# Kernel tuning notes

Hardware: AMD Instinct MI355X
Metric: run time of the kernel (lower is better)

## Reference

```python
import jax, jax.numpy as jnp
import numpy as np

N_NODES = 100000
N_EDGES = 1000000
IN_DIM = 64
OUT_DIM = 64


def setup_inputs() -> dict:
    key = jax.random.key(0)
    k1, k2, k3 = jax.random.split(key, 3)
    x = jax.random.normal(k1, (N_NODES, IN_DIM), dtype=jnp.float32)
    edge_index = jax.random.randint(k2, (2, N_EDGES), 0, N_NODES, dtype=jnp.int64)
    # PyG GCNConv linear weight [out_dim, in_dim] (glorot-ish scale) and bias
    W = jax.random.normal(k3, (OUT_DIM, IN_DIM), dtype=jnp.float32) * (1.0 / np.sqrt(IN_DIM))
    b = jnp.zeros((OUT_DIM,), dtype=jnp.float32)
    return {"x": x, "edge_index": edge_index, "W": W, "b": b}


def reference(x, edge_index, W, b):
    # GCNConv: add self-loops, symmetric deg^{-1/2} normalization,
    # linear transform, scatter-add aggregation, bias.
    # Dropout is identity in eval mode.
    N = x.shape[0]
    loop = jnp.arange(N, dtype=edge_index.dtype)
    src = jnp.concatenate([edge_index[0], loop])  # [E+N]
    dst = jnp.concatenate([edge_index[1], loop])  # [E+N]

    deg = jax.ops.segment_sum(jnp.ones_like(dst, dtype=x.dtype), dst, num_segments=N)
    dinv = jnp.where(deg > 0, jax.lax.rsqrt(deg), 0.0)  # [N]
    norm = dinv[src] * dinv[dst]                         # [E+N]

    h = x @ W.T                                          # [N, out_dim]
    msg = h[src] * norm[:, None]                         # gather + scale
    out = jax.ops.segment_sum(msg, dst, num_segments=N)  # scatter-add
    return out + b
```

## Files before the change

kernel.cpp:

```cpp
#include <hip/hip_runtime.h>

#define DIM 64
#define BIN_SHIFT 7
#define NODES_PER_BIN 128
#define MAX_BINS 1024
#define BIN_CAP 2048
#define CHUNK_EDGES 4096
#define SCATTER_THREADS 1024
#define GEMM_ROWS 128
#define FXSCALE 65536.0f
#define FXINV (1.0f / 65536.0f)
#define FXBIAS 524288u
#define MAGIC 12582912.0f
#define MAGIC_I 0x4B400000u
#define ACC_U64 33


using bf16x8 = __attribute__((ext_vector_type(8))) short;
using f32x4  = __attribute__((ext_vector_type(4))) float;

__device__ __forceinline__ unsigned short f2bf(float f) {
    unsigned u = __float_as_uint(f);
    u += 0x7fffu + ((u >> 16) & 1u);
    return (unsigned short)(u >> 16);
}
__device__ __forceinline__ float bf2f(unsigned short u) {
    return __uint_as_float((unsigned)u << 16);
}

__global__ __launch_bounds__(SCATTER_THREADS) void bin_scatter_kernel(
    const void* __restrict__ ei, int* __restrict__ gcur,
    int* __restrict__ pairs, int E, int nbins) {
    __shared__ int h1[MAX_BINS];
    __shared__ int base[MAX_BINS];
    __shared__ int s_notz;
    int tid = threadIdx.x;
    if (tid == 0) s_notz = 0;
    for (int i = tid; i < nbins; i += SCATTER_THREADS) h1[i] = 0;
    __syncthreads();
    if (((const int*)ei)[2 * tid + 1] != 0) s_notz = 1;
    __syncthreads();
    int is64 = (s_notz == 0);
    int chunk = blockIdx.x * CHUNK_EDGES;

    int ss[CHUNK_EDGES / SCATTER_THREADS], dd[CHUNK_EDGES / SCATTER_THREADS];
#pragma unroll
    for (int k = 0; k < CHUNK_EDGES / SCATTER_THREADS; ++k) {
        int i = chunk + k * SCATTER_THREADS + tid;
        if (i < E) {
            int s, d;
            if (is64) {
                s = (int)((const long long*)ei)[i];
                d = (int)((const long long*)ei)[(long long)i + E];
            } else {
                s = ((const int*)ei)[i];
                d = ((const int*)ei)[i + E];
            }
            ss[k] = s; dd[k] = d;
            atomicAdd(&h1[d >> BIN_SHIFT], 1);
        } else {
            dd[k] = -1;
        }
    }
    __syncthreads();
    for (int i = tid; i < nbins; i += SCATTER_THREADS) {
        int c = h1[i];
        base[i] = c ? (i * BIN_CAP + atomicAdd(&gcur[i], c)) : 0;
        h1[i] = 0;
    }
    __syncthreads();
#pragma unroll
    for (int k = 0; k < CHUNK_EDGES / SCATTER_THREADS; ++k) {
        if (dd[k] >= 0) {
            int bin = dd[k] >> BIN_SHIFT;
            int r = atomicAdd(&h1[bin], 1);
            int pos = base[bin] + r;
            if (pos < (bin + 1) * BIN_CAP)
                pairs[pos] = (ss[k] << BIN_SHIFT) | (dd[k] & (NODES_PER_BIN - 1));
        }
    }
}

__global__ __launch_bounds__(256) void deg_gemm_kernel(
    const float* __restrict__ x, const float* __restrict__ W,
    const int* __restrict__ pairs, const int* __restrict__ gcur,
    int* __restrict__ deg, float* __restrict__ dinv,
    unsigned short* __restrict__ h, int N) {
    __shared__ unsigned short Xs[GEMM_ROWS * 64];
    __shared__ unsigned short Ws[64 * 64];
    __shared__ int sdeg[NODES_PER_BIN];
    __shared__ float sdinv[NODES_PER_BIN];
    int tid = threadIdx.x;
    int b = blockIdx.x;
    int row0 = b << BIN_SHIFT;
    int nn = min(GEMM_ROWS, N - row0);
    int cntb = min(gcur[b], BIN_CAP);

    if (tid < NODES_PER_BIN) sdeg[tid] = 0;
#pragma unroll
    for (int u = 0; u < 2; ++u) {
        int idx = u * 256 + tid;
        int c = idx >> 3, k0 = (idx & 7) * 8;
        float4 a = *(const float4*)&W[c * 64 + k0];
        float4 bb = *(const float4*)&W[c * 64 + k0 + 4];
        bf16x8 v;
        v[0] = (short)f2bf(a.x); v[1] = (short)f2bf(a.y);
        v[2] = (short)f2bf(a.z); v[3] = (short)f2bf(a.w);
        v[4] = (short)f2bf(bb.x); v[5] = (short)f2bf(bb.y);
        v[6] = (short)f2bf(bb.z); v[7] = (short)f2bf(bb.w);
        int byteoff = c * 128 + ((k0 * 2) ^ ((c & 7) << 4));
        *(bf16x8*)((char*)Ws + byteoff) = v;
    }
    const float* xbase = x + (size_t)row0 * DIM;
#pragma unroll
    for (int u = 0; u < 4; ++u) {
        int idx = u * 256 + tid;
        int r = idx >> 3, k0 = (idx & 7) * 8;
        float4 a = make_float4(0.f, 0.f, 0.f, 0.f), bb = a;
        if (r < nn) {
            a = *(const float4*)&xbase[r * DIM + k0];
            bb = *(const float4*)&xbase[r * DIM + k0 + 4];
        }
        bf16x8 v;
        v[0] = (short)f2bf(a.x); v[1] = (short)f2bf(a.y);
        v[2] = (short)f2bf(a.z); v[3] = (short)f2bf(a.w);
        v[4] = (short)f2bf(bb.x); v[5] = (short)f2bf(bb.y);
        v[6] = (short)f2bf(bb.z); v[7] = (short)f2bf(bb.w);
        int byteoff = r * 128 + ((k0 * 2) ^ ((r & 7) << 4));
        *(bf16x8*)((char*)Xs + byteoff) = v;
    }
    __syncthreads();
    const int* pb = pairs + b * BIN_CAP;
    for (int i = tid; i < cntb; i += 256)
        atomicAdd(&sdeg[pb[i] & (NODES_PER_BIN - 1)], 1);
    __syncthreads();
    if (tid < NODES_PER_BIN) {
        int d = sdeg[tid];
        float dv = rsqrtf((float)(d + 1));
        sdinv[tid] = dv;
        if (tid < nn) {
            deg[row0 + tid] = d;
            dinv[row0 + tid] = dv;
        }
    }
    __syncthreads();

    int w = tid >> 6, l = tid & 63;
    int lm = l & 15, kg = l >> 4;
    f32x4 acc[2][4] = {};
#pragma unroll
    for (int ks = 0; ks < 2; ++ks) {
        int kbyte = ks * 64 + kg * 16;
        int r0g = 32 * w + lm;
        int r1g = 32 * w + 16 + lm;
        bf16x8 a0 = *(const bf16x8*)((const char*)Xs + r0g * 128 + (kbyte ^ ((r0g & 7) << 4)));
        bf16x8 a1 = *(const bf16x8*)((const char*)Xs + r1g * 128 + (kbyte ^ ((r1g & 7) << 4)));
#pragma unroll
        for (int nt = 0; nt < 4; ++nt) {
            int ng = nt * 16 + lm;
            bf16x8 bv = *(const bf16x8*)((const char*)Ws + ng * 128 + (kbyte ^ ((ng & 7) << 4)));
            acc[0][nt] = __builtin_amdgcn_mfma_f32_16x16x32_bf16(a0, bv, acc[0][nt], 0, 0, 0);
            acc[1][nt] = __builtin_amdgcn_mfma_f32_16x16x32_bf16(a1, bv, acc[1][nt], 0, 0, 0);
        }
    }
#pragma unroll
    for (int mt = 0; mt < 2; ++mt) {
#pragma unroll
        for (int j = 0; j < 4; ++j) {
            int rl = 32 * w + 16 * mt + (l >> 4) * 4 + j;
            if (rl < nn) {
                float dv = sdinv[rl];
                size_t rowoff = (size_t)(row0 + rl) * DIM;
#pragma unroll
                for (int nt = 0; nt < 4; ++nt)
                    h[rowoff + nt * 16 + lm] = f2bf(acc[mt][nt][j] * dv);
            }
        }
    }
}

__global__ __launch_bounds__(512) void aggregate_kernel(
    const unsigned short* __restrict__ h, const int* __restrict__ pairs,
    const int* __restrict__ gcur, const int* __restrict__ deg,
    const float* __restrict__ dinv, const float* __restrict__ bias,
    float* __restrict__ out, int N) {
    __shared__ unsigned long long acc[NODES_PER_BIN * ACC_U64];
    int b = blockIdx.x;
    int tid = threadIdx.x;
    int cnt = min(gcur[b], BIN_CAP);
    int node0 = b << BIN_SHIFT;
    int nn = min(NODES_PER_BIN, N - node0);

    for (int i = tid; i < NODES_PER_BIN * ACC_U64; i += 512) acc[i] = 0ULL;
    __syncthreads();

    int wave = tid >> 6, lane = tid & 63;
    int g = lane >> 4;
    int fq = lane & 15;
    const int* pb = pairs + b * BIN_CAP;
    int dummy = N << BIN_SHIFT;

    for (int j0 = 32 * wave; j0 < cnt; j0 += 256) {
        int pk[8]; bool vd[8];
#pragma unroll
        for (int u = 0; u < 8; ++u) {
            int e = j0 + 4 * u + g;
            vd[u] = (e < cnt);
            pk[u] = vd[u] ? pb[e] : dummy;
        }
        ushort4 r[8];
#pragma unroll
        for (int u = 0; u < 8; ++u)
            r[u] = *(const ushort4*)(h + (size_t)(pk[u] >> BIN_SHIFT) * DIM + 4 * fq);
#pragma unroll
        for (int u = 0; u < 8; ++u) {
            unsigned q0 = __float_as_uint(fmaf(bf2f(r[u].x), FXSCALE, MAGIC)) - (MAGIC_I - FXBIAS);
            unsigned q1 = __float_as_uint(fmaf(bf2f(r[u].y), FXSCALE, MAGIC)) - (MAGIC_I - FXBIAS);
            unsigned q2 = __float_as_uint(fmaf(bf2f(r[u].z), FXSCALE, MAGIC)) - (MAGIC_I - FXBIAS);
            unsigned q3 = __float_as_uint(fmaf(bf2f(r[u].w), FXSCALE, MAGIC)) - (MAGIC_I - FXBIAS);
            if (vd[u]) {
                unsigned long long* ar =
                    &acc[(pk[u] & (NODES_PER_BIN - 1)) * ACC_U64 + 2 * fq];
                atomicAdd(&ar[0], (unsigned long long)q0 | ((unsigned long long)q1 << 32));
                atomicAdd(&ar[1], (unsigned long long)q2 | ((unsigned long long)q3 << 32));
            }
        }
    }
    __syncthreads();

    const int* accd = (const int*)acc;
    float bl = bias[lane];
    for (int n0 = wave; n0 < nn; n0 += 8) {
        int gn = node0 + n0;
        int dgn = deg[gn];
        float di = dinv[gn];
        unsigned q = (unsigned)accd[n0 * (2 * ACC_U64) + lane];
        int sfx = (int)(q - (unsigned)dgn * FXBIAS);
        float sum = (float)sfx * FXINV;
        float self = bf2f(h[(size_t)gn * DIM + lane]);
        out[(size_t)gn * DIM + lane] = (sum + self) * di + bl;
    }
}

extern "C" void kernel_launch(void* const* d_in, const int* in_sizes, int n_in,
                              void* d_out, int out_size, void* d_ws, size_t ws_size,
                              hipStream_t stream) {
    const float* x = (const float*)d_in[0];
    const void* ei = d_in[1];
    const float* W = (const float*)d_in[2];
    const float* b = (const float*)d_in[3];
    float* out = (float*)d_out;

    int N = in_sizes[0] / DIM;
    int E = in_sizes[1] / 2;
    int nbins = (N + NODES_PER_BIN - 1) >> BIN_SHIFT;

    char* ws = (char*)d_ws;
    auto align256 = [](size_t v) { return (v + 255) & ~(size_t)255; };
    size_t off = 0;
    int* gcur = (int*)(ws + off);              off = align256(off + (size_t)MAX_BINS * 4);
    int* deg  = (int*)(ws + off);              off = align256(off + (size_t)(N + 1) * 4);
    float* dinv = (float*)(ws + off);          off = align256(off + (size_t)(N + 1) * 4);
    int* pairs = (int*)(ws + off);             off = align256(off + ((size_t)nbins * BIN_CAP + 64) * 4);
    unsigned short* h = (unsigned short*)(ws + off); off = align256(off + (size_t)(N + 1) * DIM * 2);

    int nchunks = (E + CHUNK_EDGES - 1) / CHUNK_EDGES;
    int gemmblocks = nbins;

    hipMemsetAsync(gcur, 0, (size_t)MAX_BINS * 4, stream);
    bin_scatter_kernel<<<nchunks, SCATTER_THREADS, 0, stream>>>(ei, gcur, pairs, E, nbins);
    deg_gemm_kernel<<<gemmblocks, 256, 0, stream>>>(x, W, pairs, gcur, deg, dinv, h, N);
    aggregate_kernel<<<nbins, 512, 0, stream>>>(h, pairs, gcur, deg, dinv, b, out, N);
}
```

Measured before the change: 128.6 us.

## Replace fixed-point LDS atomics with per-bin CSR sort and register accumulation

```diff
diff --git a/kernel.cpp b/kernel.cpp
--- a/kernel.cpp
+++ b/kernel.cpp
@@ -8,12 +8,7 @@
 #define CHUNK_EDGES 4096
 #define SCATTER_THREADS 1024
 #define GEMM_ROWS 128
-#define FXSCALE 65536.0f
-#define FXINV (1.0f / 65536.0f)
-#define FXBIAS 524288u
-#define MAGIC 12582912.0f
-#define MAGIC_I 0x4B400000u
-#define ACC_U64 33
+#define GCUR_STRIDE 16
 
 
 using bf16x8 = __attribute__((ext_vector_type(8))) short;
@@ -65,7 +60,7 @@
     __syncthreads();
     for (int i = tid; i < nbins; i += SCATTER_THREADS) {
         int c = h1[i];
-        base[i] = c ? (i * BIN_CAP + atomicAdd(&gcur[i], c)) : 0;
+        base[i] = c ? (i * BIN_CAP + atomicAdd(&gcur[i * GCUR_STRIDE], c)) : 0;
         h1[i] = 0;
     }
     __syncthreads();
@@ -84,7 +79,6 @@
 __global__ __launch_bounds__(256) void deg_gemm_kernel(
     const float* __restrict__ x, const float* __restrict__ W,
     const int* __restrict__ pairs, const int* __restrict__ gcur,
-    int* __restrict__ deg, float* __restrict__ dinv,
     unsigned short* __restrict__ h, int N) {
     __shared__ unsigned short Xs[GEMM_ROWS * 64];
     __shared__ unsigned short Ws[64 * 64];
@@ -94,7 +88,7 @@
     int b = blockIdx.x;
     int row0 = b << BIN_SHIFT;
     int nn = min(GEMM_ROWS, N - row0);
-    int cntb = min(gcur[b], BIN_CAP);
+    int cntb = min(gcur[b * GCUR_STRIDE], BIN_CAP);
 
     if (tid < NODES_PER_BIN) sdeg[tid] = 0;
 #pragma unroll
@@ -134,15 +128,8 @@
     for (int i = tid; i < cntb; i += 256)
         atomicAdd(&sdeg[pb[i] & (NODES_PER_BIN - 1)], 1);
     __syncthreads();
-    if (tid < NODES_PER_BIN) {
-        int d = sdeg[tid];
-        float dv = rsqrtf((float)(d + 1));
-        sdinv[tid] = dv;
-        if (tid < nn) {
-            deg[row0 + tid] = d;
-            dinv[row0 + tid] = dv;
-        }
-    }
+    if (tid < NODES_PER_BIN)
+        sdinv[tid] = rsqrtf((float)(sdeg[tid] + 1));
     __syncthreads();
 
     int w = tid >> 6, l = tid & 63;
@@ -181,64 +168,82 @@
 
 __global__ __launch_bounds__(512) void aggregate_kernel(
     const unsigned short* __restrict__ h, const int* __restrict__ pairs,
-    const int* __restrict__ gcur, const int* __restrict__ deg,
-    const float* __restrict__ dinv, const float* __restrict__ bias,
+    const int* __restrict__ gcur, const float* __restrict__ bias,
     float* __restrict__ out, int N) {
-    __shared__ unsigned long long acc[NODES_PER_BIN * ACC_U64];
+    __shared__ int rp[NODES_PER_BIN + 1];
+    __shared__ int cur[NODES_PER_BIN];
+    __shared__ int ssrc[BIN_CAP];
     int b = blockIdx.x;
     int tid = threadIdx.x;
-    int cnt = min(gcur[b], BIN_CAP);
+    int cnt = min(gcur[b * GCUR_STRIDE], BIN_CAP);
     int node0 = b << BIN_SHIFT;
     int nn = min(NODES_PER_BIN, N - node0);
 
-    for (int i = tid; i < NODES_PER_BIN * ACC_U64; i += 512) acc[i] = 0ULL;
-    __syncthreads();
-
-    int wave = tid >> 6, lane = tid & 63;
-    int g = lane >> 4;
-    int fq = lane & 15;
+    if (tid < NODES_PER_BIN) cur[tid] = 0;
+    __syncthreads();
     const int* pb = pairs + b * BIN_CAP;
-    int dummy = N << BIN_SHIFT;
-
-    for (int j0 = 32 * wave; j0 < cnt; j0 += 256) {
-        int pk[8]; bool vd[8];
-#pragma unroll
-        for (int u = 0; u < 8; ++u) {
-            int e = j0 + 4 * u + g;
-            vd[u] = (e < cnt);
-            pk[u] = vd[u] ? pb[e] : dummy;
-        }
-        ushort4 r[8];
-#pragma unroll
-        for (int u = 0; u < 8; ++u)
-            r[u] = *(const ushort4*)(h + (size_t)(pk[u] >> BIN_SHIFT) * DIM + 4 * fq);
-#pragma unroll
-        for (int u = 0; u < 8; ++u) {
-            unsigned q0 = __float_as_uint(fmaf(bf2f(r[u].x), FXSCALE, MAGIC)) - (MAGIC_I - FXBIAS);
-            unsigned q1 = __float_as_uint(fmaf(bf2f(r[u].y), FXSCALE, MAGIC)) - (MAGIC_I - FXBIAS);
-            unsigned q2 = __float_as_uint(fmaf(bf2f(r[u].z), FXSCALE, MAGIC)) - (MAGIC_I - FXBIAS);
-            unsigned q3 = __float_as_uint(fmaf(bf2f(r[u].w), FXSCALE, MAGIC)) - (MAGIC_I - FXBIAS);
-            if (vd[u]) {
-                unsigned long long* ar =
-                    &acc[(pk[u] & (NODES_PER_BIN - 1)) * ACC_U64 + 2 * fq];
-                atomicAdd(&ar[0], (unsigned long long)q0 | ((unsigned long long)q1 << 32));
-                atomicAdd(&ar[1], (unsigned long long)q2 | ((unsigned long long)q3 << 32));
-            }
-        }
-    }
-    __syncthreads();
-
-    const int* accd = (const int*)acc;
-    float bl = bias[lane];
-    for (int n0 = wave; n0 < nn; n0 += 8) {
-        int gn = node0 + n0;
-        int dgn = deg[gn];
-        float di = dinv[gn];
-        unsigned q = (unsigned)accd[n0 * (2 * ACC_U64) + lane];
-        int sfx = (int)(q - (unsigned)dgn * FXBIAS);
-        float sum = (float)sfx * FXINV;
-        float self = bf2f(h[(size_t)gn * DIM + lane]);
-        out[(size_t)gn * DIM + lane] = (sum + self) * di + bl;
+    int pk[4]; int np = 0;
+    for (int i = tid; i < cnt; i += 512) {
+        int p = pb[i];
+        pk[np++] = p;
+        atomicAdd(&cur[p & (NODES_PER_BIN - 1)], 1);
+    }
+    __syncthreads();
+    if (tid < NODES_PER_BIN) rp[tid + 1] = cur[tid];
+    if (tid == 0) rp[0] = 0;
+    __syncthreads();
+#pragma unroll
+    for (int s = 1; s < NODES_PER_BIN; s <<= 1) {
+        int v = 0;
+        if (tid < NODES_PER_BIN && tid >= s) v = rp[tid + 1 - s];
+        __syncthreads();
+        if (tid < NODES_PER_BIN && tid >= s) rp[tid + 1] += v;
+        __syncthreads();
+    }
+    if (tid < NODES_PER_BIN) cur[tid] = rp[tid];
+    __syncthreads();
+#pragma unroll 4
+    for (int k = 0; k < np; ++k) {
+        int r = atomicAdd(&cur[pk[k] & (NODES_PER_BIN - 1)], 1);
+        ssrc[r] = pk[k] >> BIN_SHIFT;
+    }
+    __syncthreads();
+
+    int grp = tid >> 4, fl = tid & 15;
+    float4 bl = *(const float4*)&bias[4 * fl];
+#pragma unroll 1
+    for (int k = 0; k < 4; ++k) {
+        int n = 4 * grp + k;
+        if (n >= nn) continue;
+        int s = rp[n], e = rp[n + 1];
+        float a0 = 0.f, a1 = 0.f, a2 = 0.f, a3 = 0.f;
+        int j = s;
+        for (; j + 4 <= e; j += 4) {
+            int s0 = ssrc[j], s1 = ssrc[j + 1], s2 = ssrc[j + 2], s3 = ssrc[j + 3];
+            ushort4 r0 = *(const ushort4*)(h + (size_t)s0 * DIM + 4 * fl);
+            ushort4 r1 = *(const ushort4*)(h + (size_t)s1 * DIM + 4 * fl);
+            ushort4 r2 = *(const ushort4*)(h + (size_t)s2 * DIM + 4 * fl);
+            ushort4 r3 = *(const ushort4*)(h + (size_t)s3 * DIM + 4 * fl);
+            a0 += (bf2f(r0.x) + bf2f(r1.x)) + (bf2f(r2.x) + bf2f(r3.x));
+            a1 += (bf2f(r0.y) + bf2f(r1.y)) + (bf2f(r2.y) + bf2f(r3.y));
+            a2 += (bf2f(r0.z) + bf2f(r1.z)) + (bf2f(r2.z) + bf2f(r3.z));
+            a3 += (bf2f(r0.w) + bf2f(r1.w)) + (bf2f(r2.w) + bf2f(r3.w));
+        }
+        for (; j < e; ++j) {
+            int s0 = ssrc[j];
+            ushort4 r0 = *(const ushort4*)(h + (size_t)s0 * DIM + 4 * fl);
+            a0 += bf2f(r0.x); a1 += bf2f(r0.y);
+            a2 += bf2f(r0.z); a3 += bf2f(r0.w);
+        }
+        int gn = node0 + n;
+        ushort4 sh = *(const ushort4*)(h + (size_t)gn * DIM + 4 * fl);
+        float di = rsqrtf((float)(e - s + 1));
+        float4 o;
+        o.x = (a0 + bf2f(sh.x)) * di + bl.x;
+        o.y = (a1 + bf2f(sh.y)) * di + bl.y;
+        o.z = (a2 + bf2f(sh.z)) * di + bl.z;
+        o.w = (a3 + bf2f(sh.w)) * di + bl.w;
+        *(float4*)&out[(size_t)gn * DIM + 4 * fl] = o;
     }
 }
 
@@ -258,17 +263,14 @@
     char* ws = (char*)d_ws;
     auto align256 = [](size_t v) { return (v + 255) & ~(size_t)255; };
     size_t off = 0;
-    int* gcur = (int*)(ws + off);              off = align256(off + (size_t)MAX_BINS * 4);
-    int* deg  = (int*)(ws + off);              off = align256(off + (size_t)(N + 1) * 4);
-    float* dinv = (float*)(ws + off);          off = align256(off + (size_t)(N + 1) * 4);
+    int* gcur = (int*)(ws + off);              off = align256(off + (size_t)MAX_BINS * GCUR_STRIDE * 4);
     int* pairs = (int*)(ws + off);             off = align256(off + ((size_t)nbins * BIN_CAP + 64) * 4);
     unsigned short* h = (unsigned short*)(ws + off); off = align256(off + (size_t)(N + 1) * DIM * 2);
 
     int nchunks = (E + CHUNK_EDGES - 1) / CHUNK_EDGES;
-    int gemmblocks = nbins;
-
-    hipMemsetAsync(gcur, 0, (size_t)MAX_BINS * 4, stream);
+
+    hipMemsetAsync(gcur, 0, (size_t)MAX_BINS * GCUR_STRIDE * 4, stream);
     bin_scatter_kernel<<<nchunks, SCATTER_THREADS, 0, stream>>>(ei, gcur, pairs, E, nbins);
-    deg_gemm_kernel<<<gemmblocks, 256, 0, stream>>>(x, W, pairs, gcur, deg, dinv, h, N);
-    aggregate_kernel<<<nbins, 512, 0, stream>>>(h, pairs, gcur, deg, dinv, b, out, N);
-}
+    deg_gemm_kernel<<<nbins, 256, 0, stream>>>(x, W, pairs, gcur, h, N);
+    aggregate_kernel<<<nbins, 512, 0, stream>>>(h, pairs, gcur, b, out, N);
+}
```

Measured after the change: 135.9 us. 5.7% more time.
